# Optimization experiments

Measured on AMD Instinct MI355X. Metric: run time of the kernel, lower is better.

The kernel has to match this reference:

```python
import jax, jax.numpy as jnp
import numpy as np

B, S, D, H = 4, 2048, 1024, 16
DK = D // H


def setup_inputs() -> dict:
    key = jax.random.key(0)
    ks = jax.random.split(key, 9)
    x = jax.random.normal(ks[0], (B, S, D), dtype=jnp.float32)
    scale = 1.0 / np.sqrt(D)
    wq = jax.random.normal(ks[1], (D, D), dtype=jnp.float32) * scale
    wk = jax.random.normal(ks[2], (D, D), dtype=jnp.float32) * scale
    wv = jax.random.normal(ks[3], (D, D), dtype=jnp.float32) * scale
    wo = jax.random.normal(ks[4], (D, D), dtype=jnp.float32) * scale
    bq = jax.random.normal(ks[5], (D,), dtype=jnp.float32) * 0.01
    bk = jax.random.normal(ks[6], (D,), dtype=jnp.float32) * 0.01
    bv = jax.random.normal(ks[7], (D,), dtype=jnp.float32) * 0.01
    bo = jax.random.normal(ks[8], (D,), dtype=jnp.float32) * 0.01
    # causal mask: True where scores should be masked to -inf (j > i)
    mask = jnp.triu(jnp.ones((S, S), dtype=bool), k=1)[None, None, :, :]
    return {"x": x, "wq": wq, "bq": bq, "wk": wk, "bk": bk,
            "wv": wv, "bv": bv, "wo": wo, "bo": bo, "mask": mask}


def reference(x, wq, bq, wk, bk, wv, bv, wo, bo, mask):
    b, s, _ = x.shape
    # projections
    q = (x @ wq + bq).reshape(b, s, H, DK).transpose(0, 2, 1, 3)  # [B,H,S,DK]
    k = (x @ wk + bk).reshape(b, s, H, DK).transpose(0, 2, 1, 3)
    v = (x @ wv + bv).reshape(b, s, H, DK).transpose(0, 2, 1, 3)
    scores = jnp.einsum("bhqd,bhkd->bhqk", q, k) / np.sqrt(DK)
    scores = jnp.where(mask, -jnp.inf, scores)
    attn = jax.nn.softmax(scores, axis=-1)  # dropout p=0.0 -> identity
    out = jnp.einsum("bhqk,bhkd->bhqd", attn, v)
    out = out.transpose(0, 2, 1, 3).reshape(b, s, D)
    return out @ wo + bo
```

## Files before the change

### kernel.cpp

```cpp
#include <hip/hip_runtime.h>


typedef __attribute__((ext_vector_type(8))) short short8;
typedef __attribute__((ext_vector_type(4))) float floatx4;
typedef __attribute__((ext_vector_type(4))) unsigned short ushort4v;

#define SCLF (0.125f * 1.44269504f)

__device__ __forceinline__ unsigned short f2bf(float f) {
    unsigned int u = __float_as_uint(f);
    unsigned int r = (u + 0x7fffu + ((u >> 16) & 1u)) >> 16;
    return (unsigned short)r;
}

__device__ __forceinline__ unsigned int pk2bf(float lo, float hi) {
    return __builtin_amdgcn_perm(__float_as_uint(hi), __float_as_uint(lo), 0x07060302u);
}

__device__ __forceinline__ void gll16(const unsigned short* g, unsigned short* l) {
    __builtin_amdgcn_global_load_lds(
        (const __attribute__((address_space(1))) unsigned int*)g,
        (__attribute__((address_space(3))) unsigned int*)l, 16, 0, 0);
}

__device__ __forceinline__ void xcd_tile4(int nx, int& m0, int& n0) {
    int lid = blockIdx.y * nx + blockIdx.x;
    int grp = lid & 7;
    int inner = lid >> 3;
    int my = grp * 4 + inner / nx;
    int mx = inner % nx;
    m0 = my * 256;
    n0 = mx * 256;
}

__global__ void cvtx_kernel(const float* __restrict__ x, unsigned short* __restrict__ xb) {
    int i = (blockIdx.x * 256 + threadIdx.x) * 4;
    float4 v = *(const float4*)&x[i];
    ushort4v o;
    o.x = f2bf(v.x); o.y = f2bf(v.y); o.z = f2bf(v.z); o.w = f2bf(v.w);
    *(ushort4v*)&xb[i] = o;
}

__global__ void wtrans_kernel(const float* __restrict__ wq, const float* __restrict__ wk,
                              const float* __restrict__ wv, const float* __restrict__ wo,
                              unsigned short* __restrict__ wtbase) {
    __shared__ float t[32][33];
    int z = blockIdx.z;
    const float* w = (z == 0) ? wq : (z == 1) ? wk : (z == 2) ? wv : wo;
    unsigned short* wt = wtbase + ((long)z << 20);
    int kb = blockIdx.y * 32, nb = blockIdx.x * 32;
    int col = threadIdx.x & 31, rw = threadIdx.x >> 5;
#pragma unroll
    for (int i = 0; i < 4; i++) {
        int row = rw + i * 8;
        t[row][col] = w[(kb + row) * 1024 + nb + col];
    }
    __syncthreads();
#pragma unroll
    for (int i = 0; i < 4; i++) {
        int row = rw + i * 8;
        wt[(nb + row) * 1024 + kb + col] = f2bf(t[col][row]);
    }
}

#define ASZ (256 * 64)
#define BUFSZ (2 * ASZ)

__device__ __forceinline__ short8 ldsr(const unsigned short* p) { return *(const short8*)p; }

template <bool SW>
__device__ __forceinline__ void gemm_core256sq(const unsigned short* __restrict__ A,
                                               const unsigned short* __restrict__ Bt,
                                               unsigned short* lds,
                                               int m0, int n0, floatx4 (&acc)[8][4]) {
    const int K = 1024, NT = 16;
    int tid = threadIdx.x;
    int lane = tid & 63, wave = tid >> 6;
    int wm = wave >> 2, wn = wave & 3;
    int quad = lane >> 4, l15 = lane & 15, l7 = l15 & 7;
    int rsub = lane >> 3;
    int gl = (lane & 7) ^ rsub;

    floatx4 zero4 = {0.f, 0.f, 0.f, 0.f};
#pragma unroll
    for (int i = 0; i < 8; i++)
#pragma unroll
        for (int j = 0; j < 4; j++) acc[i][j] = zero4;

    auto stageA = [&](int kt, int half) {
        const unsigned short* Ag = A + (long)m0 * K + kt * 64;
        unsigned short* as = lds + (kt & 1) * BUFSZ;
#pragma unroll
        for (int p = 0; p < 2; p++) {
            int chunk = half * 16 + wave * 2 + p;
            gll16(&Ag[(chunk * 8 + rsub) * K + gl * 8], &as[chunk * 512 + lane * 8]);
        }
    };
    auto stageB = [&](int kt, int half) {
        const unsigned short* Bg = Bt + (long)n0 * K + kt * 64;
        unsigned short* bs = lds + (kt & 1) * BUFSZ + ASZ;
#pragma unroll
        for (int p = 0; p < 2; p++) {
            int chunk = half * 16 + wave * 2 + p;
            gll16(&Bg[(chunk * 8 + rsub) * K + gl * 8], &bs[chunk * 512 + lane * 8]);
        }
    };

    stageA(0, 0); stageA(0, 1); stageB(0, 0); stageB(0, 1);
    stageB(1, 0); stageA(1, 0); stageB(1, 1);
    asm volatile("s_waitcnt vmcnt(6)" ::: "memory");
    __builtin_amdgcn_s_barrier();
    asm volatile("" ::: "memory");

    short8 af[4][2], b0[2][2], b1[2][2];

    for (int kt = 0; kt < NT; kt++) {
        const unsigned short* as = lds + (kt & 1) * BUFSZ;
        const unsigned short* bs = as + ASZ;

#pragma unroll
        for (int i = 0; i < 4; i++) {
            int r = wm * 128 + i * 16 + l15;
            af[i][0] = ldsr(&as[r * 64 + ((quad ^ l7) * 8)]);
            af[i][1] = ldsr(&as[r * 64 + (((4 + quad) ^ l7) * 8)]);
        }
#pragma unroll
        for (int j = 0; j < 2; j++) {
            int r = wn * 64 + j * 16 + l15;
            b0[j][0] = ldsr(&bs[r * 64 + ((quad ^ l7) * 8)]);
            b0[j][1] = ldsr(&bs[r * 64 + (((4 + quad) ^ l7) * 8)]);
        }
        if (kt + 1 < NT) stageA(kt + 1, 1);
        asm volatile("" ::: "memory");
        __builtin_amdgcn_s_barrier();
        asm volatile("s_waitcnt lgkmcnt(0)" ::: "memory");
        __builtin_amdgcn_sched_barrier(0);
        __builtin_amdgcn_s_setprio(1);
#pragma unroll
        for (int i = 0; i < 4; i++)
#pragma unroll
            for (int j = 0; j < 2; j++)
#pragma unroll
                for (int kk = 0; kk < 2; kk++)
                    acc[i][j] = SW
                        ? __builtin_amdgcn_mfma_f32_16x16x32_bf16(b0[j][kk], af[i][kk], acc[i][j], 0, 0, 0)
                        : __builtin_amdgcn_mfma_f32_16x16x32_bf16(af[i][kk], b0[j][kk], acc[i][j], 0, 0, 0);
        __builtin_amdgcn_s_setprio(0);
        asm volatile("" ::: "memory");
        __builtin_amdgcn_s_barrier();
        asm volatile("" ::: "memory");

#pragma unroll
        for (int j = 0; j < 2; j++) {
            int r = wn * 64 + (2 + j) * 16 + l15;
            b1[j][0] = ldsr(&bs[r * 64 + ((quad ^ l7) * 8)]);
            b1[j][1] = ldsr(&bs[r * 64 + (((4 + quad) ^ l7) * 8)]);
        }
        asm volatile("" ::: "memory");
        __builtin_amdgcn_s_barrier();
        asm volatile("s_waitcnt lgkmcnt(0)" ::: "memory");
        __builtin_amdgcn_sched_barrier(0);
        __builtin_amdgcn_s_setprio(1);
#pragma unroll
        for (int i = 0; i < 4; i++)
#pragma unroll
            for (int j = 0; j < 2; j++)
#pragma unroll
                for (int kk = 0; kk < 2; kk++)
                    acc[i][2 + j] = SW
                        ? __builtin_amdgcn_mfma_f32_16x16x32_bf16(b1[j][kk], af[i][kk], acc[i][2 + j], 0, 0, 0)
                        : __builtin_amdgcn_mfma_f32_16x16x32_bf16(af[i][kk], b1[j][kk], acc[i][2 + j], 0, 0, 0);
        __builtin_amdgcn_s_setprio(0);
        asm volatile("" ::: "memory");
        __builtin_amdgcn_s_barrier();
        asm volatile("" ::: "memory");

#pragma unroll
        for (int i = 0; i < 4; i++) {
            int r = wm * 128 + 64 + i * 16 + l15;
            af[i][0] = ldsr(&as[r * 64 + ((quad ^ l7) * 8)]);
            af[i][1] = ldsr(&as[r * 64 + (((4 + quad) ^ l7) * 8)]);
        }
        if (kt + 2 < NT) stageB(kt + 2, 0);
        asm volatile("" ::: "memory");
        __builtin_amdgcn_s_barrier();
        asm volatile("s_waitcnt lgkmcnt(0)" ::: "memory");
        __builtin_amdgcn_sched_barrier(0);
        __builtin_amdgcn_s_setprio(1);
#pragma unroll
        for (int i = 0; i < 4; i++)
#pragma unroll
            for (int j = 0; j < 2; j++)
#pragma unroll
                for (int kk = 0; kk < 2; kk++)
                    acc[4 + i][2 + j] = SW
                        ? __builtin_amdgcn_mfma_f32_16x16x32_bf16(b1[j][kk], af[i][kk], acc[4 + i][2 + j], 0, 0, 0)
                        : __builtin_amdgcn_mfma_f32_16x16x32_bf16(af[i][kk], b1[j][kk], acc[4 + i][2 + j], 0, 0, 0);
        __builtin_amdgcn_s_setprio(0);
        asm volatile("" ::: "memory");
        __builtin_amdgcn_s_barrier();
        asm volatile("" ::: "memory");

        if (kt + 2 < NT) { stageA(kt + 2, 0); stageB(kt + 2, 1); }
        __builtin_amdgcn_s_setprio(1);
#pragma unroll
        for (int i = 0; i < 4; i++)
#pragma unroll
            for (int j = 0; j < 2; j++)
#pragma unroll
                for (int kk = 0; kk < 2; kk++)
                    acc[4 + i][j] = SW
                        ? __builtin_amdgcn_mfma_f32_16x16x32_bf16(b0[j][kk], af[i][kk], acc[4 + i][j], 0, 0, 0)
                        : __builtin_amdgcn_mfma_f32_16x16x32_bf16(af[i][kk], b0[j][kk], acc[4 + i][j], 0, 0, 0);
        __builtin_amdgcn_s_setprio(0);
        if (kt + 2 < NT) {
            asm volatile("s_waitcnt vmcnt(6)" ::: "memory");
        } else if (kt + 1 < NT) {
            asm volatile("s_waitcnt vmcnt(0)" ::: "memory");
        }
        __builtin_amdgcn_s_barrier();
        asm volatile("" ::: "memory");
    }
}

__global__ __launch_bounds__(512, 2) void proj_kernel(
    const unsigned short* __restrict__ xb, const unsigned short* __restrict__ wt,
    const float* __restrict__ bq, const float* __restrict__ bk, const float* __restrict__ bv,
    unsigned short* __restrict__ qo, unsigned short* __restrict__ ko,
    unsigned short* __restrict__ vo) {
    extern __shared__ __align__(16) unsigned short smem[];
    int m0, n0;
    xcd_tile4(12, m0, n0);
    int tid = threadIdx.x, lane = tid & 63, wave = tid >> 6;
    int wm = wave >> 2, wn = wave & 3, quad = lane >> 4, l15 = lane & 15;
    floatx4 acc[8][4];

    if (n0 < 2048) {
        gemm_core256sq<true>(xb, wt, smem, m0, n0, acc);
        int which = n0 >> 10;
        const float* bias = which ? bk : bq;
        unsigned short* dst = which ? ko : qo;
        float sc = which ? 1.0f : SCLF;
#pragma unroll
        for (int mt = 0; mt < 8; mt++)
#pragma unroll
            for (int nt = 0; nt < 4; nt++) {
                int tok = m0 + wm * 128 + mt * 16 + l15;
                int b = tok >> 11, s = tok & 2047;
                int colf = (n0 + wn * 64 + nt * 16 + quad * 4) & 1023;
                float4 bb = *(const float4*)&bias[colf];
                int h = colf >> 6, dk = colf & 63;
                ushort4v o;
                o.x = f2bf((acc[mt][nt][0] + bb.x) * sc);
                o.y = f2bf((acc[mt][nt][1] + bb.y) * sc);
                o.z = f2bf((acc[mt][nt][2] + bb.z) * sc);
                o.w = f2bf((acc[mt][nt][3] + bb.w) * sc);
                *(ushort4v*)&dst[((long)((b * 16 + h) * 2048 + s)) * 64 + dk] = o;
            }
    } else {
        gemm_core256sq<false>(xb, wt, smem, m0, n0, acc);
#pragma unroll
        for (int mt = 0; mt < 8; mt++)
#pragma unroll
            for (int nt = 0; nt < 4; nt++) {
                int tok0 = m0 + wm * 128 + mt * 16 + quad * 4;
                int b = tok0 >> 11, s = tok0 & 2047;
                int colf = (n0 & 1023) + wn * 64 + nt * 16 + l15;
                int h = colf >> 6, dk = colf & 63;
                float bb = bv[colf];
                ushort4v o;
                o.x = f2bf(acc[mt][nt][0] + bb);
                o.y = f2bf(acc[mt][nt][1] + bb);
                o.z = f2bf(acc[mt][nt][2] + bb);
                o.w = f2bf(acc[mt][nt][3] + bb);
                *(ushort4v*)&vo[((long)((b * 16 + h) * 64 + dk)) * 2048 + s] = o;
            }
    }
}

__global__ __launch_bounds__(512, 2) void gemm_out_kernel(
    const unsigned short* __restrict__ ob, const unsigned short* __restrict__ wto,
    const float* __restrict__ bo, float* __restrict__ out) {
    extern __shared__ __align__(16) unsigned short smem[];
    int m0, n0;
    xcd_tile4(4, m0, n0);
    int tid = threadIdx.x, lane = tid & 63, wave = tid >> 6;
    int wm = wave >> 2, wn = wave & 3, quad = lane >> 4, l15 = lane & 15;
    floatx4 acc[8][4];
    gemm_core256sq<true>(ob, wto, smem, m0, n0, acc);

#pragma unroll
    for (int mt = 0; mt < 8; mt++)
#pragma unroll
        for (int nt = 0; nt < 4; nt++) {
            int tok = m0 + wm * 128 + mt * 16 + l15;
            int cg = n0 + wn * 64 + nt * 16 + quad * 4;
            float4 bb = *(const float4*)&bo[cg];
            float4 o;
            o.x = acc[mt][nt][0] + bb.x;
            o.y = acc[mt][nt][1] + bb.y;
            o.z = acc[mt][nt][2] + bb.z;
            o.w = acc[mt][nt][3] + bb.w;
            *(float4*)&out[(long)tok * 1024 + cg] = o;
        }
}

__device__ __forceinline__ void stage_kv(const unsigned short* __restrict__ Kg,
                                         const unsigned short* __restrict__ Vg,
                                         unsigned short* Ks, unsigned short* Vs,
                                         int lane, int wave) {
    int rsub = lane >> 3;
    int g = (lane & 7) ^ rsub;
#pragma unroll
    for (int p = 0; p < 2; p++) {
        int chunk = wave * 2 + p;
        int r = chunk * 8 + rsub;
        gll16(&Kg[r * 64 + g * 8], &Ks[chunk * 512]);
        gll16(&Vg[r * 2048 + g * 8], &Vs[chunk * 512]);
    }
}

__global__ __launch_bounds__(256, 4) void attn_kernel(
    const unsigned short* __restrict__ Q, const unsigned short* __restrict__ Kk,
    const unsigned short* __restrict__ Vt, unsigned short* __restrict__ O) {
    __shared__ __align__(16) unsigned short Ks[2][8 * 512];
    __shared__ __align__(16) unsigned short Vs[2][8 * 512];
    __shared__ __align__(16) unsigned short Ps[4 * 16 * 64];

    int bid = blockIdx.x;
    int qt = 15 - (bid >> 6);
    int bh = bid & 63;
    int q0 = qt * 128;
    long base = (long)bh * 2048 * 64;
    long vbase = (long)bh * 64 * 2048;
    int tid = threadIdx.x, lane = tid & 63, wave = tid >> 6;
    int quad = lane >> 4, l15 = lane & 15, l7 = l15 & 7;

    short8 qfA[2], qfB[2];
    int qrA = q0 + wave * 16 + l15;
    int qrB = qrA + 64;
    qfA[0] = *(const short8*)&Q[base + qrA * 64 + quad * 8];
    qfA[1] = *(const short8*)&Q[base + qrA * 64 + 32 + quad * 8];
    qfB[0] = *(const short8*)&Q[base + qrB * 64 + quad * 8];
    qfB[1] = *(const short8*)&Q[base + qrB * 64 + 32 + quad * 8];

    float lA = 0.f, lB = 0.f;
    floatx4 oA[4], oB[4];
    floatx4 zero4 = {0.f, 0.f, 0.f, 0.f};
#pragma unroll
    for (int st = 0; st < 4; st++) { oA[st] = zero4; oB[st] = zero4; }

    unsigned short* myP = &Ps[(wave * 16) * 64];
    int pw_off = l15 * 64 + (quad & 1) * 4;
    int pr0 = l15 * 64 + ((quad ^ l7) * 8);
    int pr1 = l15 * 64 + (((4 + quad) ^ l7) * 8);

    int ktmax = 2 * qt + 1;
    stage_kv(&Kk[base], &Vt[vbase], Ks[0], Vs[0], lane, wave);
    __syncthreads();

    for (int kt = 0; kt <= ktmax; kt++) {
        int cur = kt & 1;
        if (kt < ktmax)
            stage_kv(&Kk[base + (long)(kt + 1) * 64 * 64], &Vt[vbase + (kt + 1) * 64],
                     Ks[cur ^ 1], Vs[cur ^ 1], lane, wave);
        bool doA = (kt < ktmax);
        bool maskA = (kt == ktmax - 1);
        bool maskB = (kt == ktmax);

        floatx4 saA[4], saB[4];
#pragma unroll
        for (int st = 0; st < 4; st++) {
            int row = st * 16 + l15;
            short8 kf0 = ldsr(&Ks[cur][row * 64 + ((quad ^ l7) * 8)]);
            short8 kf1 = ldsr(&Ks[cur][row * 64 + (((4 + quad) ^ l7) * 8)]);
            saB[st] = __builtin_amdgcn_mfma_f32_16x16x32_bf16(kf0, qfB[0], zero4, 0, 0, 0);
            saB[st] = __builtin_amdgcn_mfma_f32_16x16x32_bf16(kf1, qfB[1], saB[st], 0, 0, 0);
            if (doA) {
                saA[st] = __builtin_amdgcn_mfma_f32_16x16x32_bf16(kf0, qfA[0], zero4, 0, 0, 0);
                saA[st] = __builtin_amdgcn_mfma_f32_16x16x32_bf16(kf1, qfA[1], saA[st], 0, 0, 0);
            }
        }

        int kg0 = kt * 64 + quad * 4;
        short8 pfB0, pfB1, pfA0, pfA1;
        {
            float p[4][4];
#pragma unroll
            for (int st = 0; st < 4; st++)
#pragma unroll
                for (int r = 0; r < 4; r++)
                    p[st][r] = __builtin_amdgcn_exp2f(saB[st][r]);
            if (maskB) {
#pragma unroll
                for (int st = 0; st < 4; st++)
#pragma unroll
                    for (int r = 0; r < 4; r++)
                        if (kg0 + st * 16 + r > qrB) p[st][r] = 0.f;
            }
            float rs = 0.f;
#pragma unroll
            for (int st = 0; st < 4; st++) {
                rs += p[st][0] + p[st][1] + p[st][2] + p[st][3];
                uint2 pw;
                pw.x = pk2bf(p[st][0], p[st][1]);
                pw.y = pk2bf(p[st][2], p[st][3]);
                *(uint2*)&myP[pw_off + (((st * 2 + (quad >> 1)) ^ l7) * 8)] = pw;
            }
            rs += __shfl_xor(rs, 16, 64);
            rs += __shfl_xor(rs, 32, 64);
            lB += rs;
            pfB0 = ldsr(&myP[pr0]);
            pfB1 = ldsr(&myP[pr1]);
        }
        if (doA) {
            float p[4][4];
#pragma unroll
            for (int st = 0; st < 4; st++)
#pragma unroll
                for (int r = 0; r < 4; r++)
                    p[st][r] = __builtin_amdgcn_exp2f(saA[st][r]);
            if (maskA) {
#pragma unroll
                for (int st = 0; st < 4; st++)
#pragma unroll
                    for (int r = 0; r < 4; r++)
                        if (kg0 + st * 16 + r > qrA) p[st][r] = 0.f;
            }
            float rs = 0.f;
#pragma unroll
            for (int st = 0; st < 4; st++) {
                rs += p[st][0] + p[st][1] + p[st][2] + p[st][3];
                uint2 pw;
                pw.x = pk2bf(p[st][0], p[st][1]);
                pw.y = pk2bf(p[st][2], p[st][3]);
                *(uint2*)&myP[pw_off + (((st * 2 + (quad >> 1)) ^ l7) * 8)] = pw;
            }
            rs += __shfl_xor(rs, 16, 64);
            rs += __shfl_xor(rs, 32, 64);
            lA += rs;
            pfA0 = ldsr(&myP[pr0]);
            pfA1 = ldsr(&myP[pr1]);
        }

#pragma unroll
        for (int st = 0; st < 4; st++) {
            int row = st * 16 + l15;
            short8 vf0 = ldsr(&Vs[cur][row * 64 + ((quad ^ l7) * 8)]);
            short8 vf1 = ldsr(&Vs[cur][row * 64 + (((4 + quad) ^ l7) * 8)]);
            oB[st] = __builtin_amdgcn_mfma_f32_16x16x32_bf16(vf0, pfB0, oB[st], 0, 0, 0);
            oB[st] = __builtin_amdgcn_mfma_f32_16x16x32_bf16(vf1, pfB1, oB[st], 0, 0, 0);
            if (doA) {
                oA[st] = __builtin_amdgcn_mfma_f32_16x16x32_bf16(vf0, pfA0, oA[st], 0, 0, 0);
                oA[st] = __builtin_amdgcn_mfma_f32_16x16x32_bf16(vf1, pfA1, oA[st], 0, 0, 0);
            }
        }
        __syncthreads();
    }

    int b = bh >> 4, h = bh & 15;
    float invA = 1.f / lA, invB = 1.f / lB;
#pragma unroll
    for (int st = 0; st < 4; st++) {
        uint2 ov;
        ov.x = pk2bf(oA[st][0] * invA, oA[st][1] * invA);
        ov.y = pk2bf(oA[st][2] * invA, oA[st][3] * invA);
        *(uint2*)&O[((long)(b * 2048 + qrA)) * 1024 + h * 64 + st * 16 + quad * 4] = ov;
        uint2 ow;
        ow.x = pk2bf(oB[st][0] * invB, oB[st][1] * invB);
        ow.y = pk2bf(oB[st][2] * invB, oB[st][3] * invB);
        *(uint2*)&O[((long)(b * 2048 + qrB)) * 1024 + h * 64 + st * 16 + quad * 4] = ow;
    }
}

extern "C" void kernel_launch(void* const* d_in, const int* in_sizes, int n_in,
                              void* d_out, int out_size, void* d_ws, size_t ws_size,
                              hipStream_t stream) {
    const float* x  = (const float*)d_in[0];
    const float* wq = (const float*)d_in[1];
    const float* bq = (const float*)d_in[2];
    const float* wk = (const float*)d_in[3];
    const float* bk = (const float*)d_in[4];
    const float* wv = (const float*)d_in[5];
    const float* bv = (const float*)d_in[6];
    const float* wo = (const float*)d_in[7];
    const float* bo = (const float*)d_in[8];

    char* w = (char*)d_ws;
    unsigned short* xb  = (unsigned short*)w;
    unsigned short* wtq = (unsigned short*)(w + (16u << 20));
    unsigned short* wto = wtq + (3u << 20);
    unsigned short* qb  = wto + (1u << 20);
    unsigned short* kb  = qb + (8u << 20);
    unsigned short* vb  = kb + (8u << 20);
    unsigned short* ob  = vb + (8u << 20);

    cvtx_kernel<<<8192, 256, 0, stream>>>(x, xb);
    wtrans_kernel<<<dim3(32, 32, 4), 256, 0, stream>>>(wq, wk, wv, wo, wtq);
    proj_kernel<<<dim3(12, 32), 512, 128 * 1024, stream>>>(xb, wtq, bq, bk, bv, qb, kb, vb);
    attn_kernel<<<1024, 256, 0, stream>>>(qb, kb, vb, ob);
    gemm_out_kernel<<<dim3(4, 32), 512, 128 * 1024, stream>>>(ob, wto, bo, (float*)d_out);
}
```

Before: 275.3 us.

## Split V projection and use 256x128 triple-buffered GEMM tiles for V and output

Splits the fused QKV projection into a Q/K kernel using the existing 256x256 core and a separate V kernel. The V kernel and the output GEMM use a new 256x128-tile core with a three-stage LDS pipeline (144 KB). The output GEMM grid doubles from 128 to 256 blocks, which is meant to fill more CUs on the 256-CU device and hide load latency. The cost is an extra kernel launch, less operand reuse per tile, and a larger LDS footprint that can limit how many blocks share a CU.

Result: faster. 258.2 us (-6.2%).

```diff
diff --git a/kernel.cpp b/kernel.cpp
--- a/kernel.cpp
+++ b/kernel.cpp
@@ -23,7 +23,7 @@
         (__attribute__((address_space(3))) unsigned int*)l, 16, 0, 0);
 }
 
-__device__ __forceinline__ void xcd_tile4(int nx, int& m0, int& n0) {
+__device__ __forceinline__ void xcd_tile_sq(int nx, int& m0, int& n0) {
     int lid = blockIdx.y * nx + blockIdx.x;
     int grp = lid & 7;
     int inner = lid >> 3;
@@ -31,6 +31,16 @@
     int mx = inner % nx;
     m0 = my * 256;
     n0 = mx * 256;
+}
+
+__device__ __forceinline__ void xcd_tile_hw(int nx, int& m0, int& n0) {
+    int lid = blockIdx.y * nx + blockIdx.x;
+    int grp = lid & 7;
+    int inner = lid >> 3;
+    int my = grp * 4 + (inner & 3);
+    int mx = inner >> 2;
+    m0 = my * 256;
+    n0 = mx * 128;
 }
 
 __global__ void cvtx_kernel(const float* __restrict__ x, unsigned short* __restrict__ xb) {
@@ -63,10 +73,10 @@
     }
 }
 
-#define ASZ (256 * 64)
-#define BUFSZ (2 * ASZ)
-
 __device__ __forceinline__ short8 ldsr(const unsigned short* p) { return *(const short8*)p; }
+
+#define ASQ (256 * 64)
+#define BUFSQ (2 * ASQ)
 
 template <bool SW>
 __device__ __forceinline__ void gemm_core256sq(const unsigned short* __restrict__ A,
@@ -89,7 +99,7 @@
 
     auto stageA = [&](int kt, int half) {
         const unsigned short* Ag = A + (long)m0 * K + kt * 64;
-        unsigned short* as = lds + (kt & 1) * BUFSZ;
+        unsigned short* as = lds + (kt & 1) * BUFSQ;
 #pragma unroll
         for (int p = 0; p < 2; p++) {
             int chunk = half * 16 + wave * 2 + p;
@@ -98,7 +108,7 @@
     };
     auto stageB = [&](int kt, int half) {
         const unsigned short* Bg = Bt + (long)n0 * K + kt * 64;
-        unsigned short* bs = lds + (kt & 1) * BUFSZ + ASZ;
+        unsigned short* bs = lds + (kt & 1) * BUFSQ + ASQ;
 #pragma unroll
         for (int p = 0; p < 2; p++) {
             int chunk = half * 16 + wave * 2 + p;
@@ -115,8 +125,8 @@
     short8 af[4][2], b0[2][2], b1[2][2];
 
     for (int kt = 0; kt < NT; kt++) {
-        const unsigned short* as = lds + (kt & 1) * BUFSZ;
-        const unsigned short* bs = as + ASZ;
+        const unsigned short* as = lds + (kt & 1) * BUFSQ;
+        const unsigned short* bs = as + ASQ;
 
 #pragma unroll
         for (int i = 0; i < 4; i++) {
@@ -223,59 +233,179 @@
     }
 }
 
-__global__ __launch_bounds__(512, 2) void proj_kernel(
+#define A3 (256 * 64)
+#define B3 (128 * 64)
+#define BUF3 (A3 + B3)
+
+template <bool SW>
+__device__ __forceinline__ void gemm_core256(const unsigned short* __restrict__ A,
+                                             const unsigned short* __restrict__ Bt,
+                                             unsigned short* lds,
+                                             int m0, int n0, floatx4 (&acc)[8][2]) {
+    const int K = 1024, NT = 16;
+    int tid = threadIdx.x;
+    int lane = tid & 63, wave = tid >> 6;
+    int wm = wave >> 2, wn = wave & 3;
+    int quad = lane >> 4, l15 = lane & 15, l7 = l15 & 7;
+    int rsub = lane >> 3;
+    int gl = (lane & 7) ^ rsub;
+
+    floatx4 zero4 = {0.f, 0.f, 0.f, 0.f};
+#pragma unroll
+    for (int i = 0; i < 8; i++)
+#pragma unroll
+        for (int j = 0; j < 2; j++) acc[i][j] = zero4;
+
+    auto stage = [&](int kt, int b) {
+        const unsigned short* Ag = A + (long)m0 * K + kt * 64;
+        const unsigned short* Bg = Bt + (long)n0 * K + kt * 64;
+        unsigned short* as = lds + b * BUF3;
+        unsigned short* bs = as + A3;
+#pragma unroll
+        for (int p = 0; p < 4; p++) {
+            int chunk = wave * 4 + p;
+            gll16(&Ag[(chunk * 8 + rsub) * K + gl * 8], &as[chunk * 512 + lane * 8]);
+        }
+#pragma unroll
+        for (int p = 0; p < 2; p++) {
+            int chunk = wave * 2 + p;
+            gll16(&Bg[(chunk * 8 + rsub) * K + gl * 8], &bs[chunk * 512 + lane * 8]);
+        }
+    };
+
+    stage(0, 0);
+    stage(1, 1);
+    stage(2, 2);
+    asm volatile("s_waitcnt vmcnt(12)" ::: "memory");
+    __builtin_amdgcn_s_barrier();
+    asm volatile("" ::: "memory");
+
+    int buf = 0;
+    for (int kt = 0; kt < NT; kt++) {
+        const unsigned short* as = lds + buf * BUF3;
+        const unsigned short* bs = as + A3;
+        short8 bf[2][2], af[4][2], ag[4][2];
+#pragma unroll
+        for (int j = 0; j < 2; j++) {
+            int rb = wn * 32 + j * 16 + l15;
+#pragma unroll
+            for (int kk = 0; kk < 2; kk++)
+                bf[j][kk] = ldsr(&bs[rb * 64 + (((kk * 4 + quad) ^ l7) * 8)]);
+        }
+#pragma unroll
+        for (int i = 0; i < 4; i++) {
+            int r = wm * 128 + i * 16 + l15;
+#pragma unroll
+            for (int kk = 0; kk < 2; kk++)
+                af[i][kk] = ldsr(&as[r * 64 + (((kk * 4 + quad) ^ l7) * 8)]);
+        }
+        __builtin_amdgcn_s_setprio(1);
+#pragma unroll
+        for (int i = 0; i < 4; i++)
+#pragma unroll
+            for (int j = 0; j < 2; j++)
+#pragma unroll
+                for (int kk = 0; kk < 2; kk++)
+                    acc[i][j] = SW
+                        ? __builtin_amdgcn_mfma_f32_16x16x32_bf16(bf[j][kk], af[i][kk], acc[i][j], 0, 0, 0)
+                        : __builtin_amdgcn_mfma_f32_16x16x32_bf16(af[i][kk], bf[j][kk], acc[i][j], 0, 0, 0);
+        __builtin_amdgcn_s_setprio(0);
+#pragma unroll
+        for (int i = 0; i < 4; i++) {
+            int r = wm * 128 + 64 + i * 16 + l15;
+#pragma unroll
+            for (int kk = 0; kk < 2; kk++)
+                ag[i][kk] = ldsr(&as[r * 64 + (((kk * 4 + quad) ^ l7) * 8)]);
+        }
+        __builtin_amdgcn_s_setprio(1);
+#pragma unroll
+        for (int i = 0; i < 4; i++)
+#pragma unroll
+            for (int j = 0; j < 2; j++)
+#pragma unroll
+                for (int kk = 0; kk < 2; kk++)
+                    acc[4 + i][j] = SW
+                        ? __builtin_amdgcn_mfma_f32_16x16x32_bf16(bf[j][kk], ag[i][kk], acc[4 + i][j], 0, 0, 0)
+                        : __builtin_amdgcn_mfma_f32_16x16x32_bf16(ag[i][kk], bf[j][kk], acc[4 + i][j], 0, 0, 0);
+        __builtin_amdgcn_s_setprio(0);
+        asm volatile("" ::: "memory");
+        __builtin_amdgcn_s_barrier();
+        asm volatile("" ::: "memory");
+        if (kt + 3 < NT) {
+            stage(kt + 3, buf);
+            asm volatile("s_waitcnt vmcnt(12)" ::: "memory");
+        } else if (kt + 3 == NT) {
+            asm volatile("s_waitcnt vmcnt(6)" ::: "memory");
+        } else if (kt + 2 == NT) {
+            asm volatile("s_waitcnt vmcnt(0)" ::: "memory");
+        }
+        __builtin_amdgcn_s_barrier();
+        asm volatile("" ::: "memory");
+        buf = (buf == 2) ? 0 : buf + 1;
+    }
+}
+
+__global__ __launch_bounds__(512, 2) void projA_kernel(
     const unsigned short* __restrict__ xb, const unsigned short* __restrict__ wt,
-    const float* __restrict__ bq, const float* __restrict__ bk, const float* __restrict__ bv,
-    unsigned short* __restrict__ qo, unsigned short* __restrict__ ko,
-    unsigned short* __restrict__ vo) {
+    const float* __restrict__ bq, const float* __restrict__ bk,
+    unsigned short* __restrict__ qo, unsigned short* __restrict__ ko) {
     extern __shared__ __align__(16) unsigned short smem[];
     int m0, n0;
-    xcd_tile4(12, m0, n0);
+    xcd_tile_sq(8, m0, n0);
     int tid = threadIdx.x, lane = tid & 63, wave = tid >> 6;
     int wm = wave >> 2, wn = wave & 3, quad = lane >> 4, l15 = lane & 15;
     floatx4 acc[8][4];
 
-    if (n0 < 2048) {
-        gemm_core256sq<true>(xb, wt, smem, m0, n0, acc);
-        int which = n0 >> 10;
-        const float* bias = which ? bk : bq;
-        unsigned short* dst = which ? ko : qo;
-        float sc = which ? 1.0f : SCLF;
-#pragma unroll
-        for (int mt = 0; mt < 8; mt++)
-#pragma unroll
-            for (int nt = 0; nt < 4; nt++) {
-                int tok = m0 + wm * 128 + mt * 16 + l15;
-                int b = tok >> 11, s = tok & 2047;
-                int colf = (n0 + wn * 64 + nt * 16 + quad * 4) & 1023;
-                float4 bb = *(const float4*)&bias[colf];
-                int h = colf >> 6, dk = colf & 63;
-                ushort4v o;
-                o.x = f2bf((acc[mt][nt][0] + bb.x) * sc);
-                o.y = f2bf((acc[mt][nt][1] + bb.y) * sc);
-                o.z = f2bf((acc[mt][nt][2] + bb.z) * sc);
-                o.w = f2bf((acc[mt][nt][3] + bb.w) * sc);
-                *(ushort4v*)&dst[((long)((b * 16 + h) * 2048 + s)) * 64 + dk] = o;
-            }
-    } else {
-        gemm_core256sq<false>(xb, wt, smem, m0, n0, acc);
-#pragma unroll
-        for (int mt = 0; mt < 8; mt++)
-#pragma unroll
-            for (int nt = 0; nt < 4; nt++) {
-                int tok0 = m0 + wm * 128 + mt * 16 + quad * 4;
-                int b = tok0 >> 11, s = tok0 & 2047;
-                int colf = (n0 & 1023) + wn * 64 + nt * 16 + l15;
-                int h = colf >> 6, dk = colf & 63;
-                float bb = bv[colf];
-                ushort4v o;
-                o.x = f2bf(acc[mt][nt][0] + bb);
-                o.y = f2bf(acc[mt][nt][1] + bb);
-                o.z = f2bf(acc[mt][nt][2] + bb);
-                o.w = f2bf(acc[mt][nt][3] + bb);
-                *(ushort4v*)&vo[((long)((b * 16 + h) * 64 + dk)) * 2048 + s] = o;
-            }
-    }
+    gemm_core256sq<true>(xb, wt, smem, m0, n0, acc);
+    int which = n0 >> 10;
+    const float* bias = which ? bk : bq;
+    unsigned short* dst = which ? ko : qo;
+    float sc = which ? 1.0f : SCLF;
+#pragma unroll
+    for (int mt = 0; mt < 8; mt++)
+#pragma unroll
+        for (int nt = 0; nt < 4; nt++) {
+            int tok = m0 + wm * 128 + mt * 16 + l15;
+            int b = tok >> 11, s = tok & 2047;
+            int colf = (n0 + wn * 64 + nt * 16 + quad * 4) & 1023;
+            float4 bb = *(const float4*)&bias[colf];
+            int h = colf >> 6, dk = colf & 63;
+            ushort4v o;
+            o.x = f2bf((acc[mt][nt][0] + bb.x) * sc);
+            o.y = f2bf((acc[mt][nt][1] + bb.y) * sc);
+            o.z = f2bf((acc[mt][nt][2] + bb.z) * sc);
+            o.w = f2bf((acc[mt][nt][3] + bb.w) * sc);
+            *(ushort4v*)&dst[((long)((b * 16 + h) * 2048 + s)) * 64 + dk] = o;
+        }
+}
+
+__global__ __launch_bounds__(512, 2) void projB_kernel(
+    const unsigned short* __restrict__ xb, const unsigned short* __restrict__ wt,
+    const float* __restrict__ bv, unsigned short* __restrict__ vo) {
+    extern __shared__ __align__(16) unsigned short smem[];
+    int m0, n0;
+    xcd_tile_hw(8, m0, n0);
+    n0 += 2048;
+    int tid = threadIdx.x, lane = tid & 63, wave = tid >> 6;
+    int wm = wave >> 2, wn = wave & 3, quad = lane >> 4, l15 = lane & 15;
+    floatx4 acc[8][2];
+    gemm_core256<false>(xb, wt, smem, m0, n0, acc);
+#pragma unroll
+    for (int mt = 0; mt < 8; mt++)
+#pragma unroll
+        for (int nt = 0; nt < 2; nt++) {
+            int tok0 = m0 + wm * 128 + mt * 16 + quad * 4;
+            int b = tok0 >> 11, s = tok0 & 2047;
+            int colf = (n0 & 1023) + wn * 32 + nt * 16 + l15;
+            int h = colf >> 6, dk = colf & 63;
+            float bb = bv[colf];
+            ushort4v o;
+            o.x = f2bf(acc[mt][nt][0] + bb);
+            o.y = f2bf(acc[mt][nt][1] + bb);
+            o.z = f2bf(acc[mt][nt][2] + bb);
+            o.w = f2bf(acc[mt][nt][3] + bb);
+            *(ushort4v*)&vo[((long)((b * 16 + h) * 64 + dk)) * 2048 + s] = o;
+        }
 }
 
 __global__ __launch_bounds__(512, 2) void gemm_out_kernel(
@@ -283,18 +413,18 @@
     const float* __restrict__ bo, float* __restrict__ out) {
     extern __shared__ __align__(16) unsigned short smem[];
     int m0, n0;
-    xcd_tile4(4, m0, n0);
+    xcd_tile_hw(8, m0, n0);
     int tid = threadIdx.x, lane = tid & 63, wave = tid >> 6;
     int wm = wave >> 2, wn = wave & 3, quad = lane >> 4, l15 = lane & 15;
-    floatx4 acc[8][4];
-    gemm_core256sq<true>(ob, wto, smem, m0, n0, acc);
+    floatx4 acc[8][2];
+    gemm_core256<true>(ob, wto, smem, m0, n0, acc);
 
 #pragma unroll
     for (int mt = 0; mt < 8; mt++)
 #pragma unroll
-        for (int nt = 0; nt < 4; nt++) {
+        for (int nt = 0; nt < 2; nt++) {
             int tok = m0 + wm * 128 + mt * 16 + l15;
-            int cg = n0 + wn * 64 + nt * 16 + quad * 4;
+            int cg = n0 + wn * 32 + nt * 16 + quad * 4;
             float4 bb = *(const float4*)&bo[cg];
             float4 o;
             o.x = acc[mt][nt][0] + bb.x;
@@ -497,7 +627,8 @@
 
     cvtx_kernel<<<8192, 256, 0, stream>>>(x, xb);
     wtrans_kernel<<<dim3(32, 32, 4), 256, 0, stream>>>(wq, wk, wv, wo, wtq);
-    proj_kernel<<<dim3(12, 32), 512, 128 * 1024, stream>>>(xb, wtq, bq, bk, bv, qb, kb, vb);
+    projA_kernel<<<dim3(8, 32), 512, 128 * 1024, stream>>>(xb, wtq, bq, bk, qb, kb);
+    projB_kernel<<<dim3(8, 32), 512, 144 * 1024, stream>>>(xb, wtq, bv, vb);
     attn_kernel<<<1024, 256, 0, stream>>>(qb, kb, vb, ob);
-    gemm_out_kernel<<<dim3(4, 32), 512, 128 * 1024, stream>>>(ob, wto, bo, (float*)d_out);
-}
+    gemm_out_kernel<<<dim3(8, 32), 512, 144 * 1024, stream>>>(ob, wto, bo, (float*)d_out);
+}
```
